# Kernel optimization log

Measured on AMD Instinct MI355X. Metric: run time of the kernel, lower is better.

Reference implementation:

```python
import jax, jax.numpy as jnp
import numpy as np

# Module config (from init_kwargs): Occ3D-nuScenes volume
VOL_MIN = np.array([-40.0, -40.0, -1.0], dtype=np.float32)
VOXEL_SIZE = 0.4
GRID_SHAPE = (200, 200, 16)  # (vol_max - vol_min) / voxel_size
K = 6          # fixed per-gaussian window; covers radii <= 0.6m (bbox span <= 5 voxels)
N_GAUSS = 32768
N_DIMS = 16


def setup_inputs() -> dict:
    key = jax.random.key(0)
    k1, k2, k3, k4, k5 = jax.random.split(key, 5)
    # Means strictly inside the volume with 1m margin so bboxes stay in-grid.
    lo = jnp.array([-39.0, -39.0, 0.0], dtype=jnp.float32)
    hi = jnp.array([39.0, 39.0, 4.4], dtype=jnp.float32)
    means3d = jax.random.uniform(k1, (N_GAUSS, 3), minval=lo, maxval=hi, dtype=jnp.float32)
    # SPD covariances: Q diag(s) Q^T with eigenvalues in [0.01, 0.04]
    A = jax.random.normal(k2, (N_GAUSS, 3, 3), dtype=jnp.float32)
    Q, _ = jnp.linalg.qr(A)
    s = jax.random.uniform(k3, (N_GAUSS, 3), minval=0.01, maxval=0.04, dtype=jnp.float32)
    covs = jnp.einsum('nij,nj,nkj->nik', Q, s, Q)
    opacities = jax.random.uniform(k4, (N_GAUSS,), dtype=jnp.float32)
    features = jax.random.normal(k5, (N_GAUSS, N_DIMS), dtype=jnp.float32)
    return {"means3d": means3d, "covs": covs, "opacities": opacities, "features": features}


def reference(means3d, covs, opacities, features):
    N, D = features.shape
    dim_x, dim_y, dim_z = GRID_SHAPE
    total = dim_x * dim_y * dim_z
    vol_min = jnp.asarray(VOL_MIN)

    inv_covs = jnp.linalg.inv(covs)                                  # [N,3,3]
    radii = 3.0 * jnp.sqrt(jnp.diagonal(covs, axis1=-2, axis2=-1))   # [N,3]

    # Bounding box in voxel indices (trunc toward zero, like the triton .to(int32))
    s = (means3d - radii - vol_min) / VOXEL_SIZE
    e = (means3d + radii - vol_min) / VOXEL_SIZE
    start = jnp.maximum(0, s.astype(jnp.int32))                      # [N,3]
    end = jnp.minimum(jnp.array(GRID_SHAPE, jnp.int32), e.astype(jnp.int32) + 1)

    offs = jnp.arange(K, dtype=jnp.int32)
    ix = start[:, 0:1] + offs   # [N,K]
    iy = start[:, 1:2] + offs
    iz = start[:, 2:3] + offs
    mask = ((ix < end[:, 0:1])[:, :, None, None]
            & (iy < end[:, 1:2])[:, None, :, None]
            & (iz < end[:, 2:3])[:, None, None, :])                  # [N,K,K,K]

    # Voxel-corner minus mean offsets (matches kernel: x*vs + vol_min - m)
    px = ix.astype(means3d.dtype) * VOXEL_SIZE + vol_min[0] - means3d[:, 0:1]  # [N,K]
    py = iy.astype(means3d.dtype) * VOXEL_SIZE + vol_min[1] - means3d[:, 1:2]
    pz = iz.astype(means3d.dtype) * VOXEL_SIZE + vol_min[2] - means3d[:, 2:3]
    d = jnp.stack(jnp.broadcast_arrays(px[:, :, None, None],
                                       py[:, None, :, None],
                                       pz[:, None, None, :]), axis=-1)  # [N,K,K,K,3]

    mahal = jnp.einsum('nxyzi,nij,nxyzj->nxyz', d, inv_covs, d)      # [N,K,K,K]
    density = opacities[:, None, None, None] * jnp.exp(-0.5 * mahal)
    density = jnp.where(mask, density, 0.0)

    flat_idx = (ix[:, :, None, None] * (dim_y * dim_z)
                + iy[:, None, :, None] * dim_z
                + iz[:, None, None, :])                               # [N,K,K,K]
    idx = flat_idx.reshape(-1)

    grid_density = jnp.zeros((total,), density.dtype).at[idx].add(density.reshape(-1))

    contrib = density[..., None] * features[:, None, None, None, :]   # [N,K,K,K,D]
    grid_feats = jnp.zeros((total, D), density.dtype).at[:, -1].set(1e-5)
    grid_feats = grid_feats.at[idx].add(contrib.reshape(-1, D))
    grid_feats = grid_feats / jnp.clip(grid_density, 1e-6, None)[:, None]

    return grid_density.reshape(GRID_SHAPE), grid_feats.reshape(*GRID_SHAPE, D)
```

## Files before the change

### kernel.cpp

```cpp
#include <hip/hip_runtime.h>
#include <math.h>

constexpr int   GX = 200, GY = 200, GZ = 16;
constexpr int   TOTAL = GX * GY * GZ;
constexpr int   ND = 16;
constexpr int   KW = 6;
constexpr float VS = 0.4f;
constexpr float VMINX = -40.0f, VMINY = -40.0f, VMINZ = -1.0f;

constexpr int   TS = 4;
constexpr int   TSZ = 8;
constexpr int   TX = 50, TY = 50, TZ = 2;
constexpr int   NT = TX * TY * TZ;
constexpr int   RS = 20;
constexpr int   CAP = 128;
constexpr int   BR  = 12;
constexpr float NHL2E = -0.72134752044448170f;

typedef float v2f __attribute__((ext_vector_type(2)));


__device__ __forceinline__ unsigned bf16_rne(float x) {
    unsigned u = __float_as_uint(x);
    return (u + 0x7fffu + ((u >> 16) & 1u)) >> 16;
}

__global__ __launch_bounds__(64) void gv_rec(
    const float* __restrict__ means, const float* __restrict__ covs,
    const float* __restrict__ opac,  const float* __restrict__ feats,
    float* __restrict__ gdata, int* __restrict__ counts, int n)
{
    int g = blockIdx.x * 64 + threadIdx.x;
    if (g >= n) return;
    if (g < NT) counts[g] = 0;
    const float* cv = covs + (size_t)g * 9;
    float a = cv[0], b = cv[1], c = cv[2], d = cv[4], e = cv[5], f = cv[8];
    float A = d * f - e * e;
    float B = c * e - b * f;
    float C = b * e - c * d;
    float invdet = 1.0f / (a * A + b * B + c * C);
    float mx = means[g * 3 + 0], my = means[g * 3 + 1], mz = means[g * 3 + 2];
    float rx = 3.0f * sqrtf(a), ry = 3.0f * sqrtf(d), rz = 3.0f * sqrtf(f);
    int sx = max(0, (int)((mx - rx - VMINX) / VS));
    int sy = max(0, (int)((my - ry - VMINY) / VS));
    int sz = max(0, (int)((mz - rz - VMINZ) / VS));
    int ex = min(GX, (int)((mx + rx - VMINX) / VS) + 1); ex = min(ex, sx + KW);
    int ey = min(GY, (int)((my + ry - VMINY) / VS) + 1); ey = min(ey, sy + KW);
    int ez = min(GZ, (int)((mz + rz - VMINZ) / VS) + 1); ez = min(ez, sz + KW);

    float rec[RS];
    rec[0] = mx; rec[1] = my; rec[2] = mz; rec[3] = opac[g];
    rec[4] = (A * invdet) * NHL2E;
    rec[5] = (B * invdet) * (2.0f * NHL2E);
    rec[6] = (C * invdet) * (2.0f * NHL2E);
    rec[7] = ((a * f - c * c) * invdet) * NHL2E;
    rec[8] = ((b * c - a * e) * invdet) * (2.0f * NHL2E);
    rec[9] = ((a * d - b * b) * invdet) * NHL2E;
    rec[10] = __int_as_float(sx | (sy << 8) | (sz << 16));
    rec[11] = __int_as_float(ex | (ey << 8) | (ez << 16));
    const float* fr = feats + (size_t)g * ND;
#pragma unroll
    for (int q = 0; q < 8; ++q) {
        unsigned lo = bf16_rne(fr[2 * q]);
        unsigned hi = bf16_rne(fr[2 * q + 1]);
        rec[12 + q] = __uint_as_float(lo | (hi << 16));
    }
    float4* dst = (float4*)(gdata + (size_t)g * RS);
#pragma unroll
    for (int q = 0; q < 5; ++q) dst[q] = ((const float4*)rec)[q];
}

__global__ __launch_bounds__(256) void gv_bin(
    const float* __restrict__ gdata, int* __restrict__ counts,
    int* __restrict__ entries, int n)
{
    int gid = blockIdx.x * 256 + threadIdx.x;
    int g = gid >> 3;
    if (g >= n) return;
    int c = gid & 7;
    int dx = c & 1, dy = (c >> 1) & 1, dz = (c >> 2) & 1;

    const float2 se = *(const float2*)(gdata + (size_t)g * RS + 10);
    int spk = __float_as_int(se.x), epk = __float_as_int(se.y);
    int sx = spk & 255, sy = (spk >> 8) & 255, sz = (spk >> 16) & 255;
    int ex = epk & 255, ey = (epk >> 8) & 255, ez = (epk >> 16) & 255;

    int tx0 = sx >> 2, nx = ((ex - 1) >> 2) - tx0;
    int ty0 = sy >> 2, ny = ((ey - 1) >> 2) - ty0;
    int tz0 = sz >> 3, nz = ((ez - 1) >> 3) - tz0;

    if (dx <= nx && dy <= ny && dz <= nz) {
        int tile = ((tx0 + dx) * TY + (ty0 + dy)) * TZ + (tz0 + dz);
        int slot = atomicAdd(&counts[tile], 1);
        if (slot < CAP) entries[(size_t)tile * CAP + slot] = g;
    }
}

__global__ __launch_bounds__(256) void gv_tile(
    const float* __restrict__ gdata, const int* __restrict__ counts,
    const int* __restrict__ entries, float* __restrict__ out)
{
    const int wv   = threadIdx.x >> 6;
    const int lane = threadIdx.x & 63;
    const int p    = blockIdx.x * 4 + wv;
    const int tz   = p & 1;
    const int rem  = p >> 1;
    const int ty   = rem % TY;
    const int tx   = rem / TY;

    __shared__ float sbuf[4][2][BR * RS];

    const int lz = lane & 3, ly = (lane >> 2) & 3, lx = lane >> 4;
    const int ix = tx * TS + lx, iy = ty * TS + ly;
    const int iz0 = tz * TSZ + lz, iz1 = iz0 + 4;
    const float pxc  = (float)ix  * VS + VMINX;
    const float pyc  = (float)iy  * VS + VMINY;
    const float pzc0 = (float)iz0 * VS + VMINZ;
    const float pzc1 = pzc0 + 4.0f * VS;

    v2f accd2 = {0.0f, 0.0f};
    v2f accf2[ND];
#pragma unroll
    for (int c = 0; c < ND; ++c) accf2[c] = (v2f){0.0f, 0.0f};
    accf2[ND - 1] = (v2f){1e-5f, 1e-5f};

    const int cnt = __builtin_amdgcn_readfirstlane(min(counts[p], CAP));
    const int* __restrict__ el = entries + (size_t)p * CAP;

    const int  rl = lane / 5;
    const int  fc = lane - rl * 5;
    const bool stager = lane < 60;
    const int  wslot = rl * RS + fc * 4;

    if (cnt > 0) {
        const int nb = (cnt + BR - 1) / BR;
        float* b0 = &sbuf[wv][0][0];
        float* b1 = &sbuf[wv][1][0];

        float4 vn; int idn2 = 0;
        if (stager) {
            int id0 = el[min(rl, cnt - 1)];
            float4 v0 = *(const float4*)(gdata + (size_t)id0 * RS + fc * 4);
            *(float4*)(b0 + wslot) = v0;
            int idn = el[min(BR + rl, cnt - 1)];
            vn = *(const float4*)(gdata + (size_t)idn * RS + fc * 4);
            idn2 = el[min(2 * BR + rl, cnt - 1)];
        }

        for (int b = 0; b < nb; ++b) {
            if (b + 1 < nb && stager) {
                float* dstb = ((b + 1) & 1) ? b1 : b0;
                *(float4*)(dstb + wslot) = vn;
                vn = *(const float4*)(gdata + (size_t)idn2 * RS + fc * 4);
                idn2 = el[min((b + 3) * BR + rl, cnt - 1)];
            }
            const float* rb = (b & 1) ? b1 : b0;
            const int rn = min(BR, cnt - b * BR);
            for (int r = 0; r < rn; ++r) {
                const float* rec = rb + r * RS;
                float4 c2 = *(const float4*)(rec + 8);
                int spk = __float_as_int(c2.z), epk = __float_as_int(c2.w);
                int sx = spk & 255, sy = (spk >> 8) & 255, sz = (spk >> 16) & 255;
                int ex = epk & 255, ey = (epk >> 8) & 255, ez = (epk >> 16) & 255;
                bool inxy = (ix >= sx) & (ix < ex) & (iy >= sy) & (iy < ey);
                bool in0 = inxy & (iz0 >= sz) & (iz0 < ez);
                bool in1 = inxy & (iz1 >= sz) & (iz1 < ez);

                float4 c0 = *(const float4*)(rec);
                float4 c1 = *(const float4*)(rec + 4);
                float px  = pxc  - c0.x;
                float py  = pyc  - c0.y;
                float pz0 = pzc0 - c0.z;
                float pz1 = pzc1 - c0.z;
                float u    = fmaf(c1.x, px, c1.y * py);
                float base = fmaf(c1.w * py, py, px * u);
                float w    = fmaf(c2.x, py, c1.z * px);
                float q0   = fmaf(fmaf(c2.y, pz0, w), pz0, base);
                float q1   = fmaf(fmaf(c2.y, pz1, w), pz1, base);
                float d0 = c0.w * __builtin_amdgcn_exp2f(q0);
                float d1 = c0.w * __builtin_amdgcn_exp2f(q1);
                d0 = in0 ? d0 : 0.0f;
                d1 = in1 ? d1 : 0.0f;
                v2f dens2 = {d0, d1};
                accd2 += dens2;

                uint4 fA = *(const uint4*)(rec + 12);
                uint4 fB = *(const uint4*)(rec + 16);
#define BFLO(u) __uint_as_float((u) << 16)
#define BFHI(u) __uint_as_float((u) & 0xffff0000u)
#define ACC2(i, f) { float fv = (f); accf2[i] += dens2 * (v2f){fv, fv}; }
                ACC2(0,  BFLO(fA.x)); ACC2(1,  BFHI(fA.x));
                ACC2(2,  BFLO(fA.y)); ACC2(3,  BFHI(fA.y));
                ACC2(4,  BFLO(fA.z)); ACC2(5,  BFHI(fA.z));
                ACC2(6,  BFLO(fA.w)); ACC2(7,  BFHI(fA.w));
                ACC2(8,  BFLO(fB.x)); ACC2(9,  BFHI(fB.x));
                ACC2(10, BFLO(fB.y)); ACC2(11, BFHI(fB.y));
                ACC2(12, BFLO(fB.z)); ACC2(13, BFHI(fB.z));
                ACC2(14, BFLO(fB.w)); ACC2(15, BFHI(fB.w));
#undef ACC2
#undef BFLO
#undef BFHI
            }
        }
    }

    const int flat0 = (ix * GY + iy) * GZ + iz0;
    out[flat0]     = accd2.x;
    out[flat0 + 4] = accd2.y;
    float inv0 = 1.0f / fmaxf(accd2.x, 1e-6f);
    float inv1 = 1.0f / fmaxf(accd2.y, 1e-6f);
    float4* fo0 = (float4*)(out + TOTAL + (size_t)flat0 * ND);
    float4* fo1 = (float4*)(out + TOTAL + (size_t)(flat0 + 4) * ND);
#pragma unroll
    for (int q = 0; q < 4; ++q) {
        float4 w0, w1;
        w0.x = accf2[q * 4 + 0].x * inv0;  w1.x = accf2[q * 4 + 0].y * inv1;
        w0.y = accf2[q * 4 + 1].x * inv0;  w1.y = accf2[q * 4 + 1].y * inv1;
        w0.z = accf2[q * 4 + 2].x * inv0;  w1.z = accf2[q * 4 + 2].y * inv1;
        w0.w = accf2[q * 4 + 3].x * inv0;  w1.w = accf2[q * 4 + 3].y * inv1;
        fo0[q] = w0;
        fo1[q] = w1;
    }
}

extern "C" void kernel_launch(void* const* d_in, const int* in_sizes, int n_in,
                              void* d_out, int out_size, void* d_ws, size_t ws_size,
                              hipStream_t stream) {
    const float* means = (const float*)d_in[0];
    const float* covs  = (const float*)d_in[1];
    const float* opac  = (const float*)d_in[2];
    const float* feats = (const float*)d_in[3];
    float* out = (float*)d_out;
    const int n = in_sizes[2];

    float* gdata   = (float*)d_ws;
    int*   counts  = (int*)(gdata + (size_t)n * RS);
    int*   entries = counts + ((NT + 63) & ~63);

    gv_rec<<<(n + 63) / 64, 64, 0, stream>>>(means, covs, opac, feats,
                                             gdata, counts, n);
    gv_bin<<<(n * 8 + 255) / 256, 256, 0, stream>>>(gdata, counts, entries, n);
    gv_tile<<<NT / 4, 256, 0, stream>>>(gdata, counts, entries, out);
}
```

Measured before the change: 99.91 us.

## Merge record and binning kernels into one launch; unroll tile record loop

Fuses the per-gaussian record build and the tile binning into a single kernel split by block index. The binning half now recomputes the bounding box from means and covariances rather than waiting on the stored records, which removes the dependency between the two stages. Counter zeroing moves to a hipMemsetAsync. The inner record loop in the tile kernel is fully unrolled over the batch size, with a liveness mask in place of a variable trip count. The trade is an extra memset launch, duplicated bbox math, and wasted lanes on partial batches.

```diff
diff --git a/kernel.cpp b/kernel.cpp
--- a/kernel.cpp
+++ b/kernel.cpp
@@ -25,74 +25,81 @@
     return (u + 0x7fffu + ((u >> 16) & 1u)) >> 16;
 }
 
-__global__ __launch_bounds__(64) void gv_rec(
+__device__ __forceinline__ void bbox_of(float mx, float my, float mz,
+                                        float a, float d, float f,
+                                        int& sx, int& sy, int& sz,
+                                        int& ex, int& ey, int& ez)
+{
+    float rx = 3.0f * sqrtf(a), ry = 3.0f * sqrtf(d), rz = 3.0f * sqrtf(f);
+    sx = max(0, (int)((mx - rx - VMINX) / VS));
+    sy = max(0, (int)((my - ry - VMINY) / VS));
+    sz = max(0, (int)((mz - rz - VMINZ) / VS));
+    ex = min(GX, (int)((mx + rx - VMINX) / VS) + 1); ex = min(ex, sx + KW);
+    ey = min(GY, (int)((my + ry - VMINY) / VS) + 1); ey = min(ey, sy + KW);
+    ez = min(GZ, (int)((mz + rz - VMINZ) / VS) + 1); ez = min(ez, sz + KW);
+}
+
+__global__ __launch_bounds__(256) void gv_prep(
     const float* __restrict__ means, const float* __restrict__ covs,
     const float* __restrict__ opac,  const float* __restrict__ feats,
-    float* __restrict__ gdata, int* __restrict__ counts, int n)
+    float* __restrict__ gdata, int* __restrict__ counts,
+    int* __restrict__ entries, int n, int recBlocks)
 {
-    int g = blockIdx.x * 64 + threadIdx.x;
-    if (g >= n) return;
-    if (g < NT) counts[g] = 0;
-    const float* cv = covs + (size_t)g * 9;
-    float a = cv[0], b = cv[1], c = cv[2], d = cv[4], e = cv[5], f = cv[8];
-    float A = d * f - e * e;
-    float B = c * e - b * f;
-    float C = b * e - c * d;
-    float invdet = 1.0f / (a * A + b * B + c * C);
-    float mx = means[g * 3 + 0], my = means[g * 3 + 1], mz = means[g * 3 + 2];
-    float rx = 3.0f * sqrtf(a), ry = 3.0f * sqrtf(d), rz = 3.0f * sqrtf(f);
-    int sx = max(0, (int)((mx - rx - VMINX) / VS));
-    int sy = max(0, (int)((my - ry - VMINY) / VS));
-    int sz = max(0, (int)((mz - rz - VMINZ) / VS));
-    int ex = min(GX, (int)((mx + rx - VMINX) / VS) + 1); ex = min(ex, sx + KW);
-    int ey = min(GY, (int)((my + ry - VMINY) / VS) + 1); ey = min(ey, sy + KW);
-    int ez = min(GZ, (int)((mz + rz - VMINZ) / VS) + 1); ez = min(ez, sz + KW);
-
-    float rec[RS];
-    rec[0] = mx; rec[1] = my; rec[2] = mz; rec[3] = opac[g];
-    rec[4] = (A * invdet) * NHL2E;
-    rec[5] = (B * invdet) * (2.0f * NHL2E);
-    rec[6] = (C * invdet) * (2.0f * NHL2E);
-    rec[7] = ((a * f - c * c) * invdet) * NHL2E;
-    rec[8] = ((b * c - a * e) * invdet) * (2.0f * NHL2E);
-    rec[9] = ((a * d - b * b) * invdet) * NHL2E;
-    rec[10] = __int_as_float(sx | (sy << 8) | (sz << 16));
-    rec[11] = __int_as_float(ex | (ey << 8) | (ez << 16));
-    const float* fr = feats + (size_t)g * ND;
-#pragma unroll
-    for (int q = 0; q < 8; ++q) {
-        unsigned lo = bf16_rne(fr[2 * q]);
-        unsigned hi = bf16_rne(fr[2 * q + 1]);
-        rec[12 + q] = __uint_as_float(lo | (hi << 16));
-    }
-    float4* dst = (float4*)(gdata + (size_t)g * RS);
-#pragma unroll
-    for (int q = 0; q < 5; ++q) dst[q] = ((const float4*)rec)[q];
-}
-
-__global__ __launch_bounds__(256) void gv_bin(
-    const float* __restrict__ gdata, int* __restrict__ counts,
-    int* __restrict__ entries, int n)
-{
-    int gid = blockIdx.x * 256 + threadIdx.x;
-    int g = gid >> 3;
-    if (g >= n) return;
-    int c = gid & 7;
-    int dx = c & 1, dy = (c >> 1) & 1, dz = (c >> 2) & 1;
-
-    const float2 se = *(const float2*)(gdata + (size_t)g * RS + 10);
-    int spk = __float_as_int(se.x), epk = __float_as_int(se.y);
-    int sx = spk & 255, sy = (spk >> 8) & 255, sz = (spk >> 16) & 255;
-    int ex = epk & 255, ey = (epk >> 8) & 255, ez = (epk >> 16) & 255;
-
-    int tx0 = sx >> 2, nx = ((ex - 1) >> 2) - tx0;
-    int ty0 = sy >> 2, ny = ((ey - 1) >> 2) - ty0;
-    int tz0 = sz >> 3, nz = ((ez - 1) >> 3) - tz0;
-
-    if (dx <= nx && dy <= ny && dz <= nz) {
-        int tile = ((tx0 + dx) * TY + (ty0 + dy)) * TZ + (tz0 + dz);
-        int slot = atomicAdd(&counts[tile], 1);
-        if (slot < CAP) entries[(size_t)tile * CAP + slot] = g;
+    if ((int)blockIdx.x < recBlocks) {
+        int g = blockIdx.x * 256 + threadIdx.x;
+        if (g >= n) return;
+        const float* cv = covs + (size_t)g * 9;
+        float a = cv[0], b = cv[1], c = cv[2], d = cv[4], e = cv[5], f = cv[8];
+        float A = d * f - e * e;
+        float B = c * e - b * f;
+        float C = b * e - c * d;
+        float invdet = 1.0f / (a * A + b * B + c * C);
+        float mx = means[g * 3 + 0], my = means[g * 3 + 1], mz = means[g * 3 + 2];
+        int sx, sy, sz, ex, ey, ez;
+        bbox_of(mx, my, mz, a, d, f, sx, sy, sz, ex, ey, ez);
+
+        float rec[RS];
+        rec[0] = mx; rec[1] = my; rec[2] = mz; rec[3] = opac[g];
+        rec[4] = (A * invdet) * NHL2E;
+        rec[5] = (B * invdet) * (2.0f * NHL2E);
+        rec[6] = (C * invdet) * (2.0f * NHL2E);
+        rec[7] = ((a * f - c * c) * invdet) * NHL2E;
+        rec[8] = ((b * c - a * e) * invdet) * (2.0f * NHL2E);
+        rec[9] = ((a * d - b * b) * invdet) * NHL2E;
+        rec[10] = __int_as_float(sx | (sy << 8) | (sz << 16));
+        rec[11] = __int_as_float(ex | (ey << 8) | (ez << 16));
+        const float* fr = feats + (size_t)g * ND;
+#pragma unroll
+        for (int q = 0; q < 8; ++q) {
+            unsigned lo = bf16_rne(fr[2 * q]);
+            unsigned hi = bf16_rne(fr[2 * q + 1]);
+            rec[12 + q] = __uint_as_float(lo | (hi << 16));
+        }
+        float4* dst = (float4*)(gdata + (size_t)g * RS);
+#pragma unroll
+        for (int q = 0; q < 5; ++q) dst[q] = ((const float4*)rec)[q];
+    } else {
+        int gid = (blockIdx.x - recBlocks) * 256 + threadIdx.x;
+        int g = gid >> 3;
+        if (g >= n) return;
+        int c = gid & 7;
+        int dx = c & 1, dy = (c >> 1) & 1, dz = (c >> 2) & 1;
+
+        const float* cv = covs + (size_t)g * 9;
+        float a = cv[0], d = cv[4], f = cv[8];
+        float mx = means[g * 3 + 0], my = means[g * 3 + 1], mz = means[g * 3 + 2];
+        int sx, sy, sz, ex, ey, ez;
+        bbox_of(mx, my, mz, a, d, f, sx, sy, sz, ex, ey, ez);
+
+        int tx0 = sx >> 2, nx = ((ex - 1) >> 2) - tx0;
+        int ty0 = sy >> 2, ny = ((ey - 1) >> 2) - ty0;
+        int tz0 = sz >> 3, nz = ((ez - 1) >> 3) - tz0;
+
+        if (dx <= nx && dy <= ny && dz <= nz) {
+            int tile = ((tx0 + dx) * TY + (ty0 + dy)) * TZ + (tz0 + dz);
+            int slot = atomicAdd(&counts[tile], 1);
+            if (slot < CAP) entries[(size_t)tile * CAP + slot] = g;
+        }
     }
 }
 
@@ -155,14 +162,16 @@
                 idn2 = el[min((b + 3) * BR + rl, cnt - 1)];
             }
             const float* rb = (b & 1) ? b1 : b0;
-            const int rn = min(BR, cnt - b * BR);
-            for (int r = 0; r < rn; ++r) {
+            const int rbase = b * BR;
+#pragma unroll
+            for (int r = 0; r < BR; ++r) {
+                const bool live = (rbase + r) < cnt;
                 const float* rec = rb + r * RS;
                 float4 c2 = *(const float4*)(rec + 8);
                 int spk = __float_as_int(c2.z), epk = __float_as_int(c2.w);
                 int sx = spk & 255, sy = (spk >> 8) & 255, sz = (spk >> 16) & 255;
                 int ex = epk & 255, ey = (epk >> 8) & 255, ez = (epk >> 16) & 255;
-                bool inxy = (ix >= sx) & (ix < ex) & (iy >= sy) & (iy < ey);
+                bool inxy = (ix >= sx) & (ix < ex) & (iy >= sy) & (iy < ey) & live;
                 bool in0 = inxy & (iz0 >= sz) & (iz0 < ez);
                 bool in1 = inxy & (iz1 >= sz) & (iz1 < ez);
 
@@ -237,8 +246,11 @@
     int*   counts  = (int*)(gdata + (size_t)n * RS);
     int*   entries = counts + ((NT + 63) & ~63);
 
-    gv_rec<<<(n + 63) / 64, 64, 0, stream>>>(means, covs, opac, feats,
-                                             gdata, counts, n);
-    gv_bin<<<(n * 8 + 255) / 256, 256, 0, stream>>>(gdata, counts, entries, n);
+    const int recBlocks = (n + 255) / 256;
+    const int binBlocks = (n * 8 + 255) / 256;
+
+    hipMemsetAsync(counts, 0, NT * sizeof(int), stream);
+    gv_prep<<<recBlocks + binBlocks, 256, 0, stream>>>(
+        means, covs, opac, feats, gdata, counts, entries, n, recBlocks);
     gv_tile<<<NT / 4, 256, 0, stream>>>(gdata, counts, entries, out);
 }
```

Measured after the change: 103.4 us. +3.5%, slower.

## Double tile size in y so each lane accumulates four voxels per gaussian

Applied to the files above, without the earlier changes.

Tiles grow from 4x4x8 to 4x8x8 voxels, so each lane now handles two y positions and two z positions, four voxels per gaussian record. The per-record quadratic form is split into shared partial terms, and each staged record and decoded bf16 feature is reused across twice as many voxels. Binning uses y shift 3 and the per-tile capacity doubles to 256. This halves the number of tiles and repeated record loads per voxel. In exchange it doubles the accumulator registers, which may lower occupancy, and each tile's gaussian list grows, lengthening the serial loop per wave.

```diff
diff --git a/kernel.cpp b/kernel.cpp
--- a/kernel.cpp
+++ b/kernel.cpp
@@ -8,12 +8,13 @@
 constexpr float VS = 0.4f;
 constexpr float VMINX = -40.0f, VMINY = -40.0f, VMINZ = -1.0f;
 
-constexpr int   TS = 4;
+constexpr int   TSX = 4;
+constexpr int   TSY = 8;
 constexpr int   TSZ = 8;
-constexpr int   TX = 50, TY = 50, TZ = 2;
+constexpr int   TX = 50, TY = 25, TZ = 2;
 constexpr int   NT = TX * TY * TZ;
 constexpr int   RS = 20;
-constexpr int   CAP = 128;
+constexpr int   CAP = 256;
 constexpr int   BR  = 12;
 constexpr float NHL2E = -0.72134752044448170f;
 
@@ -86,7 +87,7 @@
     int ex = epk & 255, ey = (epk >> 8) & 255, ez = (epk >> 16) & 255;
 
     int tx0 = sx >> 2, nx = ((ex - 1) >> 2) - tx0;
-    int ty0 = sy >> 2, ny = ((ey - 1) >> 2) - ty0;
+    int ty0 = sy >> 3, ny = ((ey - 1) >> 3) - ty0;
     int tz0 = sz >> 3, nz = ((ez - 1) >> 3) - tz0;
 
     if (dx <= nx && dy <= ny && dz <= nz) {
@@ -111,18 +112,22 @@
     __shared__ float sbuf[4][2][BR * RS];
 
     const int lz = lane & 3, ly = (lane >> 2) & 3, lx = lane >> 4;
-    const int ix = tx * TS + lx, iy = ty * TS + ly;
+    const int ix  = tx * TSX + lx;
+    const int iy0 = ty * TSY + ly, iy1 = iy0 + 4;
     const int iz0 = tz * TSZ + lz, iz1 = iz0 + 4;
     const float pxc  = (float)ix  * VS + VMINX;
-    const float pyc  = (float)iy  * VS + VMINY;
+    const float pyc0 = (float)iy0 * VS + VMINY;
+    const float pyc1 = pyc0 + 4.0f * VS;
     const float pzc0 = (float)iz0 * VS + VMINZ;
     const float pzc1 = pzc0 + 4.0f * VS;
 
-    v2f accd2 = {0.0f, 0.0f};
-    v2f accf2[ND];
-#pragma unroll
-    for (int c = 0; c < ND; ++c) accf2[c] = (v2f){0.0f, 0.0f};
-    accf2[ND - 1] = (v2f){1e-5f, 1e-5f};
+    v2f accdA = {0.0f, 0.0f};
+    v2f accdB = {0.0f, 0.0f};
+    v2f accfA[ND], accfB[ND];
+#pragma unroll
+    for (int c = 0; c < ND; ++c) { accfA[c] = (v2f){0.f, 0.f}; accfB[c] = (v2f){0.f, 0.f}; }
+    accfA[ND - 1] = (v2f){1e-5f, 1e-5f};
+    accfB[ND - 1] = (v2f){1e-5f, 1e-5f};
 
     const int cnt = __builtin_amdgcn_readfirstlane(min(counts[p], CAP));
     const int* __restrict__ el = entries + (size_t)p * CAP;
@@ -162,64 +167,90 @@
                 int spk = __float_as_int(c2.z), epk = __float_as_int(c2.w);
                 int sx = spk & 255, sy = (spk >> 8) & 255, sz = (spk >> 16) & 255;
                 int ex = epk & 255, ey = (epk >> 8) & 255, ez = (epk >> 16) & 255;
-                bool inxy = (ix >= sx) & (ix < ex) & (iy >= sy) & (iy < ey);
-                bool in0 = inxy & (iz0 >= sz) & (iz0 < ez);
-                bool in1 = inxy & (iz1 >= sz) & (iz1 < ez);
+                bool inx  = (ix  >= sx) & (ix  < ex);
+                bool iny0 = (iy0 >= sy) & (iy0 < ey) & inx;
+                bool iny1 = (iy1 >= sy) & (iy1 < ey) & inx;
+                bool inz0 = (iz0 >= sz) & (iz0 < ez);
+                bool inz1 = (iz1 >= sz) & (iz1 < ez);
 
                 float4 c0 = *(const float4*)(rec);
                 float4 c1 = *(const float4*)(rec + 4);
                 float px  = pxc  - c0.x;
-                float py  = pyc  - c0.y;
-                float pz0 = pzc0 - c0.z;
-                float pz1 = pzc1 - c0.z;
-                float u    = fmaf(c1.x, px, c1.y * py);
-                float base = fmaf(c1.w * py, py, px * u);
-                float w    = fmaf(c2.x, py, c1.z * px);
-                float q0   = fmaf(fmaf(c2.y, pz0, w), pz0, base);
-                float q1   = fmaf(fmaf(c2.y, pz1, w), pz1, base);
-                float d0 = c0.w * __builtin_amdgcn_exp2f(q0);
-                float d1 = c0.w * __builtin_amdgcn_exp2f(q1);
-                d0 = in0 ? d0 : 0.0f;
-                d1 = in1 ? d1 : 0.0f;
-                v2f dens2 = {d0, d1};
-                accd2 += dens2;
+                float py0 = pyc0 - c0.y, py1 = pyc1 - c0.y;
+                float pz0 = pzc0 - c0.z, pz1 = pzc1 - c0.z;
+                float A  = c1.x * px * px;
+                float B0 = fmaf(py0, fmaf(c1.w, py0, c1.y * px), A);
+                float B1 = fmaf(py1, fmaf(c1.w, py1, c1.y * px), A);
+                float C0 = pz0 * fmaf(c2.y, pz0, c1.z * px);
+                float C1 = pz1 * fmaf(c2.y, pz1, c1.z * px);
+                float t0 = c2.x * pz0, t1 = c2.x * pz1;
+                float q00_ = fmaf(py0, t0, B0 + C0);
+                float q01_ = fmaf(py0, t1, B0 + C1);
+                float q10_ = fmaf(py1, t0, B1 + C0);
+                float q11_ = fmaf(py1, t1, B1 + C1);
+                float d00 = c0.w * __builtin_amdgcn_exp2f(q00_);
+                float d01 = c0.w * __builtin_amdgcn_exp2f(q01_);
+                float d10 = c0.w * __builtin_amdgcn_exp2f(q10_);
+                float d11 = c0.w * __builtin_amdgcn_exp2f(q11_);
+                d00 = (iny0 & inz0) ? d00 : 0.0f;
+                d01 = (iny0 & inz1) ? d01 : 0.0f;
+                d10 = (iny1 & inz0) ? d10 : 0.0f;
+                d11 = (iny1 & inz1) ? d11 : 0.0f;
+                v2f densA = {d00, d01};
+                v2f densB = {d10, d11};
+                accdA += densA;
+                accdB += densB;
 
                 uint4 fA = *(const uint4*)(rec + 12);
                 uint4 fB = *(const uint4*)(rec + 16);
 #define BFLO(u) __uint_as_float((u) << 16)
 #define BFHI(u) __uint_as_float((u) & 0xffff0000u)
-#define ACC2(i, f) { float fv = (f); accf2[i] += dens2 * (v2f){fv, fv}; }
-                ACC2(0,  BFLO(fA.x)); ACC2(1,  BFHI(fA.x));
-                ACC2(2,  BFLO(fA.y)); ACC2(3,  BFHI(fA.y));
-                ACC2(4,  BFLO(fA.z)); ACC2(5,  BFHI(fA.z));
-                ACC2(6,  BFLO(fA.w)); ACC2(7,  BFHI(fA.w));
-                ACC2(8,  BFLO(fB.x)); ACC2(9,  BFHI(fB.x));
-                ACC2(10, BFLO(fB.y)); ACC2(11, BFHI(fB.y));
-                ACC2(12, BFLO(fB.z)); ACC2(13, BFHI(fB.z));
-                ACC2(14, BFLO(fB.w)); ACC2(15, BFHI(fB.w));
-#undef ACC2
+#define ACC4(i, f) { float fv = (f); v2f fvv = {fv, fv};                    \
+                     accfA[i] += densA * fvv; accfB[i] += densB * fvv; }
+                ACC4(0,  BFLO(fA.x)); ACC4(1,  BFHI(fA.x));
+                ACC4(2,  BFLO(fA.y)); ACC4(3,  BFHI(fA.y));
+                ACC4(4,  BFLO(fA.z)); ACC4(5,  BFHI(fA.z));
+                ACC4(6,  BFLO(fA.w)); ACC4(7,  BFHI(fA.w));
+                ACC4(8,  BFLO(fB.x)); ACC4(9,  BFHI(fB.x));
+                ACC4(10, BFLO(fB.y)); ACC4(11, BFHI(fB.y));
+                ACC4(12, BFLO(fB.z)); ACC4(13, BFHI(fB.z));
+                ACC4(14, BFLO(fB.w)); ACC4(15, BFHI(fB.w));
+#undef ACC4
 #undef BFLO
 #undef BFHI
             }
         }
     }
 
-    const int flat0 = (ix * GY + iy) * GZ + iz0;
-    out[flat0]     = accd2.x;
-    out[flat0 + 4] = accd2.y;
-    float inv0 = 1.0f / fmaxf(accd2.x, 1e-6f);
-    float inv1 = 1.0f / fmaxf(accd2.y, 1e-6f);
-    float4* fo0 = (float4*)(out + TOTAL + (size_t)flat0 * ND);
-    float4* fo1 = (float4*)(out + TOTAL + (size_t)(flat0 + 4) * ND);
+    const int flat00 = (ix * GY + iy0) * GZ + iz0;
+    const int flat10 = flat00 + 4 * GZ;
+    out[flat00]     = accdA.x;
+    out[flat00 + 4] = accdA.y;
+    out[flat10]     = accdB.x;
+    out[flat10 + 4] = accdB.y;
+    float i00 = 1.0f / fmaxf(accdA.x, 1e-6f);
+    float i01 = 1.0f / fmaxf(accdA.y, 1e-6f);
+    float i10 = 1.0f / fmaxf(accdB.x, 1e-6f);
+    float i11 = 1.0f / fmaxf(accdB.y, 1e-6f);
+    float4* fo00 = (float4*)(out + TOTAL + (size_t)flat00 * ND);
+    float4* fo01 = (float4*)(out + TOTAL + (size_t)(flat00 + 4) * ND);
+    float4* fo10 = (float4*)(out + TOTAL + (size_t)flat10 * ND);
+    float4* fo11 = (float4*)(out + TOTAL + (size_t)(flat10 + 4) * ND);
 #pragma unroll
     for (int q = 0; q < 4; ++q) {
-        float4 w0, w1;
-        w0.x = accf2[q * 4 + 0].x * inv0;  w1.x = accf2[q * 4 + 0].y * inv1;
-        w0.y = accf2[q * 4 + 1].x * inv0;  w1.y = accf2[q * 4 + 1].y * inv1;
-        w0.z = accf2[q * 4 + 2].x * inv0;  w1.z = accf2[q * 4 + 2].y * inv1;
-        w0.w = accf2[q * 4 + 3].x * inv0;  w1.w = accf2[q * 4 + 3].y * inv1;
-        fo0[q] = w0;
-        fo1[q] = w1;
+        float4 w00, w01, w10, w11;
+        w00.x = accfA[q*4+0].x * i00;  w01.x = accfA[q*4+0].y * i01;
+        w00.y = accfA[q*4+1].x * i00;  w01.y = accfA[q*4+1].y * i01;
+        w00.z = accfA[q*4+2].x * i00;  w01.z = accfA[q*4+2].y * i01;
+        w00.w = accfA[q*4+3].x * i00;  w01.w = accfA[q*4+3].y * i01;
+        w10.x = accfB[q*4+0].x * i10;  w11.x = accfB[q*4+0].y * i11;
+        w10.y = accfB[q*4+1].x * i10;  w11.y = accfB[q*4+1].y * i11;
+        w10.z = accfB[q*4+2].x * i10;  w11.z = accfB[q*4+2].y * i11;
+        w10.w = accfB[q*4+3].x * i10;  w11.w = accfB[q*4+3].y * i11;
+        fo00[q] = w00;
+        fo01[q] = w01;
+        fo10[q] = w10;
+        fo11[q] = w11;
     }
 }
 
```

Measured after the change: 114.8 us. 14.9% more time.
